# Optimization experiments

Hardware: AMD Instinct MI355X
Metric: run time of the kernel (lower is better)

## Reference

```python
import jax, jax.numpy as jnp
import numpy as np

N_ATOMS = 100000
N_EDGES = 800000
ATOM_DIM = 32
BOND_DIM = 16


def setup_inputs() -> dict:
    key = jax.random.key(0)
    k1, k2, k3, k4 = jax.random.split(key, 4)
    atom_features = jax.random.normal(k1, (N_ATOMS, ATOM_DIM), dtype=jnp.float32)
    bond_features = jax.random.normal(k2, (N_EDGES, BOND_DIM), dtype=jnp.float32)
    pair_indices = jax.random.randint(k3, (N_EDGES, 2), 0, N_ATOMS, dtype=jnp.int64 if jax.config.jax_enable_x64 else jnp.int32)
    # glorot-uniform-ish kernel
    limit = np.sqrt(6.0 / (BOND_DIM + ATOM_DIM * ATOM_DIM))
    kernel = jax.random.uniform(k4, (BOND_DIM, ATOM_DIM * ATOM_DIM), dtype=jnp.float32, minval=-limit, maxval=limit)
    bias = jnp.zeros((ATOM_DIM * ATOM_DIM,), dtype=jnp.float32)
    return {"atom_features": atom_features, "bond_features": bond_features,
            "pair_indices": pair_indices, "kernel": kernel, "bias": bias}


def reference(atom_features, bond_features, pair_indices, kernel, bias):
    atom_dim = atom_features.shape[-1]
    n_atoms = atom_features.shape[0]
    # bond-conditioned per-edge transform matrices: [E, atom_dim, atom_dim]
    bt = (bond_features @ kernel + bias).reshape(-1, atom_dim, atom_dim)
    # gather neighbor atom features: [E, atom_dim]
    neigh = atom_features[pair_indices[:, 1]]
    # per-edge small matmul: messages [E, atom_dim]
    messages = jnp.einsum('eij,ej->ei', bt, neigh)
    # scatter-add to destination atoms
    aggregated = jax.ops.segment_sum(messages, pair_indices[:, 0], num_segments=n_atoms)
    return aggregated
```

## Files before the change

kernel.cpp:

```cpp
#include <hip/hip_runtime.h>
#include <hip/hip_bf16.h>

typedef __attribute__((ext_vector_type(8))) short short8;
typedef __attribute__((ext_vector_type(4))) short s16x4;
typedef __attribute__((ext_vector_type(4))) float f32x4;

#define N_ATOMS 100000
#define N_EDGES 800000
#define N_TILES (N_EDGES/16)
#define WAVE_PAIRS 2048
#define N_CHUNKS ((N_ATOMS + 255) / 256)

#define WS_MSG     0ULL
#define WS_OFFS    51200000ULL
#define WS_COUNTS  51600016ULL
#define WS_CURSOR  52000016ULL
#define WS_SLOT    52400016ULL
#define WS_PART    55600016ULL
#define WS_NEED    55602064ULL

__device__ __forceinline__ short f2bf(float x) {
    __hip_bfloat16 h = __float2bfloat16(x);
    return __builtin_bit_cast(short, h);
}
__device__ __forceinline__ float bf2f(short b) {
    unsigned u = ((unsigned)(unsigned short)b) << 16;
    return __builtin_bit_cast(float, u);
}

__global__ __launch_bounds__(256) void zero_ints(int* __restrict__ p, int n) {
    int i = blockIdx.x * 256 + threadIdx.x;
    if (i < n) p[i] = 0;
}

__global__ __launch_bounds__(256) void rank_kernel(const int2* __restrict__ pair,
                                                   int* __restrict__ counts,
                                                   int* __restrict__ slot) {
    int e = blockIdx.x * 256 + threadIdx.x;
    if (e < N_EDGES) slot[e] = atomicAdd(&counts[pair[e].x], 1);
}

__global__ __launch_bounds__(256) void scan_part(const int* __restrict__ counts,
                                                 int* __restrict__ partials) {
    const int tid = threadIdx.x;
    const int i = blockIdx.x * 256 + tid;
    int v = (i < N_ATOMS) ? counts[i] : 0;
#pragma unroll
    for (int off = 1; off < 64; off <<= 1) v += __shfl_xor(v, off);
    __shared__ int ws4[4];
    const int lane = tid & 63, wv = tid >> 6;
    if (lane == 0) ws4[wv] = v;
    __syncthreads();
    if (tid == 0) partials[blockIdx.x] = ws4[0] + ws4[1] + ws4[2] + ws4[3];
}

__global__ __launch_bounds__(512) void scan_mid(int* __restrict__ partials) {
    const int tid = threadIdx.x;
    const int lane = tid & 63, wv = tid >> 6;
    int v = (tid < N_CHUNKS) ? partials[tid] : 0;
    int inc = v;
#pragma unroll
    for (int off = 1; off < 64; off <<= 1) {
        int u = __shfl_up(inc, off);
        if (lane >= off) inc += u;
    }
    __shared__ int ws8[8];
    if (lane == 63) ws8[wv] = inc;
    __syncthreads();
    int base = 0;
#pragma unroll
    for (int k = 0; k < 8; ++k) base += (k < wv) ? ws8[k] : 0;
    if (tid < N_CHUNKS) partials[tid] = base + inc - v;
}

__global__ __launch_bounds__(256) void scan_final(const int* __restrict__ counts,
                                                  const int* __restrict__ partials,
                                                  int* __restrict__ offsets) {
    const int tid = threadIdx.x;
    const int i = blockIdx.x * 256 + tid;
    const int lane = tid & 63, wv = tid >> 6;
    int c = (i < N_ATOMS) ? counts[i] : 0;
    int inc = c;
#pragma unroll
    for (int off = 1; off < 64; off <<= 1) {
        int u = __shfl_up(inc, off);
        if (lane >= off) inc += u;
    }
    __shared__ int ws4[4];
    if (lane == 63) ws4[wv] = inc;
    __syncthreads();
    int base = partials[blockIdx.x];
#pragma unroll
    for (int k = 0; k < 4; ++k) base += (k < wv) ? ws4[k] : 0;
    const int off = base + inc - c;
    if (i < N_ATOMS) offsets[i] = off;
    if (i == N_ATOMS - 1) offsets[N_ATOMS] = off + c;
}

__global__ __launch_bounds__(256) void slot_add_kernel(const int2* __restrict__ pair,
                                                       const int* __restrict__ offsets,
                                                       int* __restrict__ slot) {
    int e = blockIdx.x * 256 + threadIdx.x;
    if (e < N_EDGES) slot[e] += offsets[pair[e].x];
}

__global__ __launch_bounds__(256, 4)
void edge_msg_kernel(const float* __restrict__ atom,
                     const float* __restrict__ bond,
                     const int2*  __restrict__ pair,
                     const float* __restrict__ kern,
                     const float* __restrict__ bias,
                     const int*   __restrict__ slot,
                     short*       __restrict__ msg)
{
    __shared__ __align__(16) short alds[17*2*512];
    __shared__ __align__(16) float blds[4][16*20];

    const int tid = threadIdx.x;
    for (int x = tid; x < 17*2*512; x += 256) {
        const int t = x & 7;
        const int l = (x >> 3) & 63;
        const int m = (x >> 9) & 1;
        const int b = x >> 10;
        const int i = m*16 + (l & 15);
        const int j = ((l >> 4) << 3) + t;
        const float v = (b < 16) ? kern[b*1024 + i*32 + j] : bias[i*32 + j];
        alds[x] = f2bf(v);
    }
    __syncthreads();

    const int wave = tid >> 6;
    const int lane = tid & 63;
    const int er   = lane & 15;
    const int jg   = lane >> 4;
    const int wid  = blockIdx.x * 4 + wave;
    const int m    = wid & 1;
    const int pid  = wid >> 1;

    short8 afr[16];
#pragma unroll
    for (int b = 0; b < 16; ++b)
        afr[b] = *(const short8*)&alds[(b*2 + m)*512 + lane*8];
    const short* afr16p = &alds[(16*2 + m)*512 + lane*8];

    const int ibase = m*16 + jg*4;

    float* bw = &blds[wave][(lane >> 2)*20 + (lane & 3)*4];
    const float* brd = &blds[wave][er*20];

    int t0 = pid;
    int2  pc = pair[t0*16 + er];
    int   sc = slot[t0*16 + er];
    f32x4 bvc = *(const f32x4*)(bond + t0*256 + lane*4);
    f32x4 n0 = *(const f32x4*)(atom + pc.y*32 + jg*8);
    f32x4 n1 = *(const f32x4*)(atom + pc.y*32 + jg*8 + 4);
    *(f32x4*)bw = bvc;

    for (int t = pid; t < N_TILES; t += WAVE_PAIRS) {
        const int tn  = t + WAVE_PAIRS;
        const int tcl = (tn < N_TILES) ? tn : (N_TILES - 1);

        const int2  pn  = pair[tcl*16 + er];
        const int   sn  = slot[tcl*16 + er];
        const f32x4 bvn = *(const f32x4*)(bond + tcl*256 + lane*4);

        const f32x4 q0 = *(const f32x4*)(brd + 0);
        const f32x4 q1 = *(const f32x4*)(brd + 4);
        const f32x4 q2 = *(const f32x4*)(brd + 8);
        const f32x4 q3 = *(const f32x4*)(brd + 12);
        const short8 af16 = *(const short8*)afr16p;

        short8 bfrag;
        bfrag[0] = f2bf(n0[0]); bfrag[1] = f2bf(n0[1]);
        bfrag[2] = f2bf(n0[2]); bfrag[3] = f2bf(n0[3]);
        bfrag[4] = f2bf(n1[0]); bfrag[5] = f2bf(n1[1]);
        bfrag[6] = f2bf(n1[2]); bfrag[7] = f2bf(n1[3]);

        float bb[16];
        bb[0]=q0[0];  bb[1]=q0[1];  bb[2]=q0[2];  bb[3]=q0[3];
        bb[4]=q1[0];  bb[5]=q1[1];  bb[6]=q1[2];  bb[7]=q1[3];
        bb[8]=q2[0];  bb[9]=q2[1];  bb[10]=q2[2]; bb[11]=q2[3];
        bb[12]=q3[0]; bb[13]=q3[1]; bb[14]=q3[2]; bb[15]=q3[3];

        f32x4 macc = {0.f,0.f,0.f,0.f};
        f32x4 z = {0.f,0.f,0.f,0.f};
#pragma unroll
        for (int b = 0; b < 16; ++b) {
            f32x4 d = __builtin_amdgcn_mfma_f32_16x16x32_bf16(afr[b], bfrag, z, 0, 0, 0);
            macc[0] = fmaf(bb[b], d[0], macc[0]);
            macc[1] = fmaf(bb[b], d[1], macc[1]);
            macc[2] = fmaf(bb[b], d[2], macc[2]);
            macc[3] = fmaf(bb[b], d[3], macc[3]);
        }
        {
            f32x4 d = __builtin_amdgcn_mfma_f32_16x16x32_bf16(af16, bfrag, z, 0, 0, 0);
            macc[0] += d[0]; macc[1] += d[1]; macc[2] += d[2]; macc[3] += d[3];
        }

        const f32x4 n0n = *(const f32x4*)(atom + pn.y*32 + jg*8);
        const f32x4 n1n = *(const f32x4*)(atom + pn.y*32 + jg*8 + 4);

        *(f32x4*)bw = bvn;

        s16x4 mv;
        mv[0] = f2bf(macc[0]); mv[1] = f2bf(macc[1]);
        mv[2] = f2bf(macc[2]); mv[3] = f2bf(macc[3]);
        *(s16x4*)&msg[sc*32 + ibase] = mv;

        pc = pn; sc = sn; n0 = n0n; n1 = n1n;
    }
}

__global__ __launch_bounds__(256) void gather_kernel(const short* __restrict__ msg,
                                                     const int* __restrict__ offsets,
                                                     float* __restrict__ out) {
    const int tid = threadIdx.x;
    const int a = blockIdx.x * 32 + (tid >> 3);
    const int sub = (tid & 7) * 4;
    if (a >= N_ATOMS) return;
    const int b0 = offsets[a], b1 = offsets[a + 1];
    f32x4 acc0 = {0.f, 0.f, 0.f, 0.f};
    f32x4 acc1 = {0.f, 0.f, 0.f, 0.f};
    int k = b0;
    for (; k + 1 < b1; k += 2) {
        s16x4 mv0 = *(const s16x4*)&msg[k*32 + sub];
        s16x4 mv1 = *(const s16x4*)&msg[(k+1)*32 + sub];
        acc0[0] += bf2f(mv0[0]); acc0[1] += bf2f(mv0[1]);
        acc0[2] += bf2f(mv0[2]); acc0[3] += bf2f(mv0[3]);
        acc1[0] += bf2f(mv1[0]); acc1[1] += bf2f(mv1[1]);
        acc1[2] += bf2f(mv1[2]); acc1[3] += bf2f(mv1[3]);
    }
    if (k < b1) {
        s16x4 mv0 = *(const s16x4*)&msg[k*32 + sub];
        acc0[0] += bf2f(mv0[0]); acc0[1] += bf2f(mv0[1]);
        acc0[2] += bf2f(mv0[2]); acc0[3] += bf2f(mv0[3]);
    }
    acc0[0] += acc1[0]; acc0[1] += acc1[1]; acc0[2] += acc1[2]; acc0[3] += acc1[3];
    *(f32x4*)&out[a*32 + sub] = acc0;
}

__global__ __launch_bounds__(256) void zero_out(f32x4* __restrict__ out) {
    int i = blockIdx.x * 256 + threadIdx.x;
    f32x4 z = {0.f, 0.f, 0.f, 0.f};
    out[i] = z;
}

__global__ __launch_bounds__(256, 4)
void edge_kernel_atomic(const float* __restrict__ atom, const float* __restrict__ bond,
                        const int2* __restrict__ pair, const float* __restrict__ kern,
                        const float* __restrict__ bias, float* __restrict__ out)
{
    __shared__ __align__(16) short alds[17*2*512];
    const int tid = threadIdx.x;
    for (int x = tid; x < 17*2*512; x += 256) {
        const int t = x & 7;
        const int l = (x >> 3) & 63;
        const int m = (x >> 9) & 1;
        const int b = x >> 10;
        const int i = m*16 + (l & 15);
        const int j = ((l >> 4) << 3) + t;
        const float v = (b < 16) ? kern[b*1024 + i*32 + j] : bias[i*32 + j];
        alds[x] = f2bf(v);
    }
    __syncthreads();
    const int wave = tid >> 6, lane = tid & 63;
    const int er = lane & 15, jg = lane >> 4;
    const int wid = blockIdx.x * 4 + wave;
    const int m = wid & 1, pid = wid >> 1;
    short8 afr[17];
#pragma unroll
    for (int b = 0; b < 17; ++b)
        afr[b] = *(const short8*)&alds[(b*2 + m)*512 + lane*8];
    const int ibase = m*16 + jg*4;
    for (int tile = pid; tile < N_TILES; tile += WAVE_PAIRS) {
        const int e = tile*16 + er;
        const int2 p = pair[e];
        const f32x4* arow = (const f32x4*)(atom + p.y * 32);
        const f32x4 n0 = arow[jg*2];
        const f32x4 n1 = arow[jg*2 + 1];
        short8 bfrag;
        bfrag[0] = f2bf(n0[0]); bfrag[1] = f2bf(n0[1]);
        bfrag[2] = f2bf(n0[2]); bfrag[3] = f2bf(n0[3]);
        bfrag[4] = f2bf(n1[0]); bfrag[5] = f2bf(n1[1]);
        bfrag[6] = f2bf(n1[2]); bfrag[7] = f2bf(n1[3]);
        const f32x4* brow = (const f32x4*)(bond + e * 16);
        const f32x4 q0 = brow[0], q1 = brow[1], q2 = brow[2], q3 = brow[3];
        float bb[17];
        bb[0]=q0[0];  bb[1]=q0[1];  bb[2]=q0[2];  bb[3]=q0[3];
        bb[4]=q1[0];  bb[5]=q1[1];  bb[6]=q1[2];  bb[7]=q1[3];
        bb[8]=q2[0];  bb[9]=q2[1];  bb[10]=q2[2]; bb[11]=q2[3];
        bb[12]=q3[0]; bb[13]=q3[1]; bb[14]=q3[2]; bb[15]=q3[3];
        bb[16]=1.0f;
        f32x4 macc = {0.f,0.f,0.f,0.f};
#pragma unroll
        for (int b = 0; b < 17; ++b) {
            f32x4 z = {0.f,0.f,0.f,0.f};
            f32x4 d = __builtin_amdgcn_mfma_f32_16x16x32_bf16(afr[b], bfrag, z, 0, 0, 0);
            macc[0] = fmaf(bb[b], d[0], macc[0]);
            macc[1] = fmaf(bb[b], d[1], macc[1]);
            macc[2] = fmaf(bb[b], d[2], macc[2]);
            macc[3] = fmaf(bb[b], d[3], macc[3]);
        }
        float* obase = out + p.x * 32 + ibase;
        atomicAdd(obase + 0, macc[0]);
        atomicAdd(obase + 1, macc[1]);
        atomicAdd(obase + 2, macc[2]);
        atomicAdd(obase + 3, macc[3]);
    }
}

extern "C" void kernel_launch(void* const* d_in, const int* in_sizes, int n_in,
                              void* d_out, int out_size, void* d_ws, size_t ws_size,
                              hipStream_t stream)
{
    (void)in_sizes; (void)n_in; (void)out_size;
    const float* atom = (const float*)d_in[0];
    const float* bond = (const float*)d_in[1];
    const int2*  pair = (const int2*)d_in[2];
    const float* kern = (const float*)d_in[3];
    const float* bias = (const float*)d_in[4];
    float* out = (float*)d_out;

    if (ws_size < WS_NEED) {
        zero_out<<<dim3(N_ATOMS*32/4/256), dim3(256), 0, stream>>>((f32x4*)out);
        edge_kernel_atomic<<<dim3(1024), dim3(256), 0, stream>>>(atom, bond, pair, kern, bias, out);
        return;
    }

    char* ws = (char*)d_ws;
    short* msg    = (short*)(ws + WS_MSG);
    int* offsets  = (int*)(ws + WS_OFFS);
    int* counts   = (int*)(ws + WS_COUNTS);
    int* slot     = (int*)(ws + WS_SLOT);
    int* partials = (int*)(ws + WS_PART);

    const int eb = (N_EDGES + 255) / 256;
    zero_ints<<<dim3((N_ATOMS + 255)/256), dim3(256), 0, stream>>>(counts, N_ATOMS);
    rank_kernel<<<dim3(eb), dim3(256), 0, stream>>>(pair, counts, slot);
    scan_part<<<dim3(N_CHUNKS), dim3(256), 0, stream>>>(counts, partials);
    scan_mid<<<dim3(1), dim3(512), 0, stream>>>(partials);
    scan_final<<<dim3(N_CHUNKS), dim3(256), 0, stream>>>(counts, partials, offsets);
    slot_add_kernel<<<dim3(eb), dim3(256), 0, stream>>>(pair, offsets, slot);
    edge_msg_kernel<<<dim3(1024), dim3(256), 0, stream>>>(atom, bond, pair, kern, bias, slot, msg);
    gather_kernel<<<dim3((N_ATOMS + 31)/32), dim3(256), 0, stream>>>(msg, offsets, out);
}
```

Measured before the change: 120.8 us.

## Pack per-edge source and slot into one int2, deepen edge prefetch pipeline

A new preprocessing kernel packs each edge's neighbor index and destination slot into one int2 array, so the edge kernel reads one stream instead of separate pair and slot arrays. The edge kernel now prefetches two tiles ahead and double-buffers the bond staging in LDS, which gives the atom gathers more time to arrive. The bias fragment moves into registers and the kernel-weight LDS region is reused for the bond buffers. Occupancy hint drops from 4 to 3 blocks per CU, trading latency hiding from more waves for more registers per wave.

```diff
diff --git a/kernel.cpp b/kernel.cpp
--- a/kernel.cpp
+++ b/kernel.cpp
@@ -14,10 +14,10 @@
 #define WS_MSG     0ULL
 #define WS_OFFS    51200000ULL
 #define WS_COUNTS  51600016ULL
-#define WS_CURSOR  52000016ULL
-#define WS_SLOT    52400016ULL
-#define WS_PART    55600016ULL
-#define WS_NEED    55602064ULL
+#define WS_EDATA   52000016ULL
+#define WS_RANK    58400016ULL
+#define WS_PART    61600016ULL
+#define WS_NEED    61602064ULL
 
 __device__ __forceinline__ short f2bf(float x) {
     __hip_bfloat16 h = __float2bfloat16(x);
@@ -35,9 +35,9 @@
 
 __global__ __launch_bounds__(256) void rank_kernel(const int2* __restrict__ pair,
                                                    int* __restrict__ counts,
-                                                   int* __restrict__ slot) {
+                                                   int* __restrict__ rank) {
     int e = blockIdx.x * 256 + threadIdx.x;
-    if (e < N_EDGES) slot[e] = atomicAdd(&counts[pair[e].x], 1);
+    if (e < N_EDGES) rank[e] = atomicAdd(&counts[pair[e].x], 1);
 }
 
 __global__ __launch_bounds__(256) void scan_part(const int* __restrict__ counts,
@@ -97,35 +97,41 @@
     if (i == N_ATOMS - 1) offsets[N_ATOMS] = off + c;
 }
 
-__global__ __launch_bounds__(256) void slot_add_kernel(const int2* __restrict__ pair,
-                                                       const int* __restrict__ offsets,
-                                                       int* __restrict__ slot) {
+__global__ __launch_bounds__(256) void edata_kernel(const int2* __restrict__ pair,
+                                                    const int* __restrict__ offsets,
+                                                    const int* __restrict__ rank,
+                                                    int2* __restrict__ edata) {
     int e = blockIdx.x * 256 + threadIdx.x;
-    if (e < N_EDGES) slot[e] += offsets[pair[e].x];
-}
-
-__global__ __launch_bounds__(256, 4)
+    if (e < N_EDGES) {
+        int2 p = pair[e];
+        int2 d;
+        d.x = p.y;
+        d.y = offsets[p.x] + rank[e];
+        edata[e] = d;
+    }
+}
+
+__global__ __launch_bounds__(256, 3)
 void edge_msg_kernel(const float* __restrict__ atom,
                      const float* __restrict__ bond,
-                     const int2*  __restrict__ pair,
                      const float* __restrict__ kern,
                      const float* __restrict__ bias,
-                     const int*   __restrict__ slot,
+                     const int2*  __restrict__ edata,
                      short*       __restrict__ msg)
 {
-    __shared__ __align__(16) short alds[17*2*512];
-    __shared__ __align__(16) float blds[4][16*20];
-
-    const int tid = threadIdx.x;
-    for (int x = tid; x < 17*2*512; x += 256) {
+    __shared__ __align__(16) char smem[32768];
+    short* klds = (short*)smem;
+    float* blds = (float*)smem;
+
+    const int tid = threadIdx.x;
+    for (int x = tid; x < 16*2*512; x += 256) {
         const int t = x & 7;
         const int l = (x >> 3) & 63;
         const int m = (x >> 9) & 1;
         const int b = x >> 10;
         const int i = m*16 + (l & 15);
         const int j = ((l >> 4) << 3) + t;
-        const float v = (b < 16) ? kern[b*1024 + i*32 + j] : bias[i*32 + j];
-        alds[x] = f2bf(v);
+        klds[x] = f2bf(kern[b*1024 + i*32 + j]);
     }
     __syncthreads();
 
@@ -140,35 +146,49 @@
     short8 afr[16];
 #pragma unroll
     for (int b = 0; b < 16; ++b)
-        afr[b] = *(const short8*)&alds[(b*2 + m)*512 + lane*8];
-    const short* afr16p = &alds[(16*2 + m)*512 + lane*8];
+        afr[b] = *(const short8*)&klds[(b*2 + m)*512 + lane*8];
+
+    short8 af16;
+    {
+        const float* bp = bias + (m*16 + er)*32 + jg*8;
+        const f32x4 z0 = *(const f32x4*)bp;
+        const f32x4 z1 = *(const f32x4*)(bp + 4);
+        af16[0]=f2bf(z0[0]); af16[1]=f2bf(z0[1]); af16[2]=f2bf(z0[2]); af16[3]=f2bf(z0[3]);
+        af16[4]=f2bf(z1[0]); af16[5]=f2bf(z1[1]); af16[6]=f2bf(z1[2]); af16[7]=f2bf(z1[3]);
+    }
+    __syncthreads();
 
     const int ibase = m*16 + jg*4;
 
-    float* bw = &blds[wave][(lane >> 2)*20 + (lane & 3)*4];
-    const float* brd = &blds[wave][er*20];
-
-    int t0 = pid;
-    int2  pc = pair[t0*16 + er];
-    int   sc = slot[t0*16 + er];
-    f32x4 bvc = *(const f32x4*)(bond + t0*256 + lane*4);
-    f32x4 n0 = *(const f32x4*)(atom + pc.y*32 + jg*8);
-    f32x4 n1 = *(const f32x4*)(atom + pc.y*32 + jg*8 + 4);
-    *(f32x4*)bw = bvc;
+    float* bwA = blds + (0*4 + wave)*320 + (lane >> 2)*20 + (lane & 3)*4;
+    float* bwB = blds + (1*4 + wave)*320 + (lane >> 2)*20 + (lane & 3)*4;
+    const float* brA = blds + (0*4 + wave)*320 + er*20;
+    const float* brB = blds + (1*4 + wave)*320 + er*20;
+
+    const int last = N_TILES - 1;
+
+    const int tA = pid;
+    const int tB = (pid + WAVE_PAIRS <= last) ? pid + WAVE_PAIRS : last;
+    int2  e0 = edata[tA*16 + er];
+    f32x4 bv0 = *(const f32x4*)(bond + tA*256 + lane*4);
+    int2  e1 = edata[tB*16 + er];
+    f32x4 bv1 = *(const f32x4*)(bond + tB*256 + lane*4);
+    f32x4 n0 = *(const f32x4*)(atom + e0.x*32 + jg*8);
+    f32x4 n1 = *(const f32x4*)(atom + e0.x*32 + jg*8 + 4);
+    *(f32x4*)bwA = bv0;
 
     for (int t = pid; t < N_TILES; t += WAVE_PAIRS) {
-        const int tn  = t + WAVE_PAIRS;
-        const int tcl = (tn < N_TILES) ? tn : (N_TILES - 1);
-
-        const int2  pn  = pair[tcl*16 + er];
-        const int   sn  = slot[tcl*16 + er];
-        const f32x4 bvn = *(const f32x4*)(bond + tcl*256 + lane*4);
-
-        const f32x4 q0 = *(const f32x4*)(brd + 0);
-        const f32x4 q1 = *(const f32x4*)(brd + 4);
-        const f32x4 q2 = *(const f32x4*)(brd + 8);
-        const f32x4 q3 = *(const f32x4*)(brd + 12);
-        const short8 af16 = *(const short8*)afr16p;
+        int tn2 = t + 2*WAVE_PAIRS; tn2 = (tn2 <= last) ? tn2 : last;
+        const int2  e2  = edata[tn2*16 + er];
+        const f32x4 bv2 = *(const f32x4*)(bond + tn2*256 + lane*4);
+
+        const f32x4 n0n = *(const f32x4*)(atom + e1.x*32 + jg*8);
+        const f32x4 n1n = *(const f32x4*)(atom + e1.x*32 + jg*8 + 4);
+
+        const f32x4 q0 = *(const f32x4*)(brA + 0);
+        const f32x4 q1 = *(const f32x4*)(brA + 4);
+        const f32x4 q2 = *(const f32x4*)(brA + 8);
+        const f32x4 q3 = *(const f32x4*)(brA + 12);
 
         short8 bfrag;
         bfrag[0] = f2bf(n0[0]); bfrag[1] = f2bf(n0[1]);
@@ -183,7 +203,7 @@
         bb[12]=q3[0]; bb[13]=q3[1]; bb[14]=q3[2]; bb[15]=q3[3];
 
         f32x4 macc = {0.f,0.f,0.f,0.f};
-        f32x4 z = {0.f,0.f,0.f,0.f};
+        const f32x4 z = {0.f,0.f,0.f,0.f};
 #pragma unroll
         for (int b = 0; b < 16; ++b) {
             f32x4 d = __builtin_amdgcn_mfma_f32_16x16x32_bf16(afr[b], bfrag, z, 0, 0, 0);
@@ -197,17 +217,16 @@
             macc[0] += d[0]; macc[1] += d[1]; macc[2] += d[2]; macc[3] += d[3];
         }
 
-        const f32x4 n0n = *(const f32x4*)(atom + pn.y*32 + jg*8);
-        const f32x4 n1n = *(const f32x4*)(atom + pn.y*32 + jg*8 + 4);
-
-        *(f32x4*)bw = bvn;
+        *(f32x4*)bwB = bv1;
 
         s16x4 mv;
         mv[0] = f2bf(macc[0]); mv[1] = f2bf(macc[1]);
         mv[2] = f2bf(macc[2]); mv[3] = f2bf(macc[3]);
-        *(s16x4*)&msg[sc*32 + ibase] = mv;
-
-        pc = pn; sc = sn; n0 = n0n; n1 = n1n;
+        *(s16x4*)&msg[(long long)e0.y*32 + ibase] = mv;
+
+        e0 = e1; e1 = e2; bv1 = bv2; n0 = n0n; n1 = n1n;
+        float* tw = bwA; bwA = bwB; bwB = tw;
+        const float* tr = brA; brA = brB; brB = tr;
     }
 }
 
@@ -331,16 +350,17 @@
     short* msg    = (short*)(ws + WS_MSG);
     int* offsets  = (int*)(ws + WS_OFFS);
     int* counts   = (int*)(ws + WS_COUNTS);
-    int* slot     = (int*)(ws + WS_SLOT);
+    int2* edata   = (int2*)(ws + WS_EDATA);
+    int* rank     = (int*)(ws + WS_RANK);
     int* partials = (int*)(ws + WS_PART);
 
     const int eb = (N_EDGES + 255) / 256;
     zero_ints<<<dim3((N_ATOMS + 255)/256), dim3(256), 0, stream>>>(counts, N_ATOMS);
-    rank_kernel<<<dim3(eb), dim3(256), 0, stream>>>(pair, counts, slot);
+    rank_kernel<<<dim3(eb), dim3(256), 0, stream>>>(pair, counts, rank);
     scan_part<<<dim3(N_CHUNKS), dim3(256), 0, stream>>>(counts, partials);
     scan_mid<<<dim3(1), dim3(512), 0, stream>>>(partials);
     scan_final<<<dim3(N_CHUNKS), dim3(256), 0, stream>>>(counts, partials, offsets);
-    slot_add_kernel<<<dim3(eb), dim3(256), 0, stream>>>(pair, offsets, slot);
-    edge_msg_kernel<<<dim3(1024), dim3(256), 0, stream>>>(atom, bond, pair, kern, bias, slot, msg);
+    edata_kernel<<<dim3(eb), dim3(256), 0, stream>>>(pair, offsets, rank, edata);
+    edge_msg_kernel<<<dim3(1024), dim3(256), 0, stream>>>(atom, bond, kern, bias, edata, msg);
     gather_kernel<<<dim3((N_ATOMS + 31)/32), dim3(256), 0, stream>>>(msg, offsets, out);
 }
```

Result: faster. 117.2 us (-3.0%).
